# Kernel optimization log

Hardware: AMD Instinct MI355X
Metric: run time of the kernel (lower is better)

Reference implementation:

```python
import jax, jax.numpy as jnp
import numpy as np

DIM = 2048
K = 8                 # top_k
M = 16                # max_transients
BIND_FRAC = 0.15
BETA = 0.05
GAMMA = 0.9
LIFETIME = 5
B, T = 64, 256

_iu, _ju = np.triu_indices(K, k=1)   # row-major: matches torch's (ii outer, jj inner) loop order
IU = jnp.asarray(_iu, jnp.int32)
JU = jnp.asarray(_ju, jnp.int32)


def _renorm(s):
    n = jnp.sqrt(jnp.sum(jnp.abs(s) ** 2, axis=-1, keepdims=True))
    return s / jnp.maximum(n, 1e-8)


def setup_inputs() -> dict:
    key = jax.random.key(0)
    ks = jax.random.split(key, 5)
    return {
        "x": jax.random.normal(ks[0], (B, T, DIM), jnp.float32),
        "tape_re": jax.random.normal(ks[1], (DIM,), jnp.float32) / np.sqrt(DIM).astype(np.float32),
        "tape_im": jax.random.normal(ks[2], (DIM,), jnp.float32) / np.sqrt(DIM).astype(np.float32),
        "eta_param": jnp.asarray(0.1, jnp.float32),
        "torque_bias_re": jax.random.normal(ks[3], (DIM,), jnp.float32) * 0.01,
        "torque_bias_im": jax.random.normal(ks[4], (DIM,), jnp.float32) * 0.01,
    }


def _per_batch(h, s, ti, tj, mre, mim, cnt, eta, tbias):
    """One timestep for one batch element. s: [D] complex64, transients: 5 arrays of [M]."""
    c = h * s                               # Hadamard reception
    _, top_idx = jax.lax.top_k(jnp.abs(c), K)
    top_c = c[top_idx]
    tm = jnp.abs(top_c)
    ph = jnp.angle(top_c)
    # co-resonance scores for the K*(K-1)/2 pairs; torch detaches via .item()
    score = jax.lax.stop_gradient(tm[IU] * tm[JU] * jnp.cos(ph[IU] - ph[JU]))
    pos = score > 0
    n_pos = jnp.sum(pos.astype(jnp.int32))
    n_bind = jnp.maximum(1, (n_pos.astype(jnp.float32) * BIND_FRAC).astype(jnp.int32))
    sorted_desc = -jnp.sort(-jnp.where(pos, score, -jnp.inf))
    theta_idx = jnp.minimum(n_bind - 1, jnp.maximum(n_pos - 1, 0))
    theta = sorted_desc[theta_idx]
    bind = (score >= theta) & (n_pos > 0)   # theta>0 so only positive scores pass

    ci = top_idx[IU]
    cj = top_idx[JU]
    prod = s[ci] * s[cj]
    mnew = jax.lax.stop_gradient(BETA * prod / jnp.maximum(jnp.abs(prod), 1e-8))  # torch detaches via .item()

    def step(tr, inp):
        ti, tj, mre, mim, cnt = tr
        ci_p, cj_p, do, mr, mi = inp
        active = cnt > 0
        match = active & (((ti == ci_p) & (tj == cj_p)) | ((ti == cj_p) & (tj == ci_p)))
        has_match = jnp.any(match)
        midx = jnp.argmax(match)
        free = ~active
        has_free = jnp.any(free)
        fidx = jnp.argmax(free)
        refresh = do & has_match
        insert = do & (~has_match) & has_free
        cnt = jnp.where(refresh, cnt.at[midx].set(LIFETIME), cnt)
        ti = jnp.where(insert, ti.at[fidx].set(ci_p), ti)
        tj = jnp.where(insert, tj.at[fidx].set(cj_p), tj)
        mre = jnp.where(insert, mre.at[fidx].set(mr), mre)
        mim = jnp.where(insert, mim.at[fidx].set(mi), mim)
        cnt = jnp.where(insert, cnt.at[fidx].set(LIFETIME), cnt)
        return (ti, tj, mre, mim, cnt), None

    (ti, tj, mre, mim, cnt), _ = jax.lax.scan(
        step, (ti, tj, mre, mim, cnt), (ci, cj, bind, mnew.real, mnew.imag))

    # decay all transients
    mre = mre * GAMMA
    mim = mim * GAMMA
    cnt = cnt - 1
    alive = (cnt > 0) & (jnp.sqrt(mre * mre + mim * mim) > 1e-6)
    cnt = jnp.where(alive, cnt, 0)
    mre = jnp.where(alive, mre, 0.0)
    mim = jnp.where(alive, mim, 0.0)

    # augment state with transients (scatter-add to both endpoints)
    s_re = s.real.at[ti].add(0.1 * mre).at[tj].add(0.1 * mre)
    s_im = s.imag.at[ti].add(0.1 * mim).at[tj].add(0.1 * mim)
    s_aug = jax.lax.complex(s_re, s_im)

    c_aug = h * s_aug
    re_c = c_aug.real
    im_c = c_aug.imag
    res_mask = ((re_c > 1e-6) & (jnp.abs(im_c) < re_c)).astype(jnp.float32)
    tor_mask = ((re_c < -1e-6) | (jnp.abs(im_c) >= jnp.abs(re_c))).astype(jnp.float32)
    orth_mask = 1.0 - res_mask - tor_mask
    update = eta * (c_aug * (1.0 - orth_mask) + tor_mask * tbias)
    s_new = _renorm(s + update)
    return s_new, ti, tj, mre, mim, cnt


def _forward(x, tape_re, tape_im, eta_param, torque_bias_re, torque_bias_im):
    Bb, Tt, D = x.shape
    s0 = _renorm(jax.lax.complex(tape_re, tape_im)[None, :])
    s0 = jnp.broadcast_to(s0, (Bb, D))
    eta = jnp.abs(eta_param)
    tbias = jax.lax.complex(torque_bias_re, torque_bias_im)
    ti0 = jnp.zeros((Bb, M), jnp.int32)
    tj0 = jnp.zeros((Bb, M), jnp.int32)
    mre0 = jnp.zeros((Bb, M), jnp.float32)
    mim0 = jnp.zeros((Bb, M), jnp.float32)
    cnt0 = jnp.zeros((Bb, M), jnp.int32)

    step_b = jax.vmap(_per_batch, in_axes=(0, 0, 0, 0, 0, 0, 0, None, None))

    def time_step(carry, h_t):
        s, ti, tj, mre, mim, cnt = carry
        s, ti, tj, mre, mim, cnt = step_b(h_t, s, ti, tj, mre, mim, cnt, eta, tbias)
        return (s, ti, tj, mre, mim, cnt), jnp.abs(s)

    _, outs = jax.lax.scan(time_step, (s0, ti0, tj0, mre0, mim0, cnt0),
                           jnp.transpose(x, (1, 0, 2)))  # [T,B,D]
    return jnp.transpose(outs, (1, 0, 2))                # [B,T,D]


def reference(x, tape_re, tape_im, eta_param, torque_bias_re, torque_bias_im):
    return _forward(x, tape_re, tape_im, eta_param, torque_bias_re, torque_bias_im)
```

## Files before the change

kernel.cpp:

```cpp
#include <hip/hip_runtime.h>
#include <math.h>

#define DIM_ 2048
#define KTOP 8
#define MSLOT 16
#define TSTEPS 256
#define NB 64
#define NTHREADS 320
#define NWORK 256
#define EPT 8

static_assert(NWORK * EPT == DIM_, "mapping");

#define DPP0(src, ctrl, rm) __builtin_amdgcn_update_dpp(0, (src), (ctrl), (rm), 0xf, true)

__device__ __forceinline__ void ced(double &a, double &b) {
  double mx = fmax(a, b);
  b = fmin(a, b);
  a = mx;
}

__device__ __forceinline__ void sort8_desc(double k[8]) {
  ced(k[0],k[1]); ced(k[2],k[3]); ced(k[4],k[5]); ced(k[6],k[7]);
  ced(k[0],k[2]); ced(k[1],k[3]); ced(k[4],k[6]); ced(k[5],k[7]);
  ced(k[1],k[2]); ced(k[5],k[6]);
  ced(k[0],k[4]); ced(k[1],k[5]); ced(k[2],k[6]); ced(k[3],k[7]);
  ced(k[2],k[4]); ced(k[3],k[5]);
  ced(k[1],k[2]); ced(k[3],k[4]); ced(k[5],k[6]);
}

template <int CTRL, int RM>
__device__ __forceinline__ void merge_level(double k[8]) {
  double b[8];
#pragma unroll
  for (int i = 0; i < 8; i++) {
    int lo = DPP0(__double2loint(k[i]), CTRL, RM);
    int hi = DPP0(__double2hiint(k[i]), CTRL, RM);
    b[i] = __hiloint2double(hi, lo);
  }
#pragma unroll
  for (int i = 0; i < 8; i++) k[i] = fmax(k[i], b[7 - i]);
  ced(k[0],k[4]); ced(k[1],k[5]); ced(k[2],k[6]); ced(k[3],k[7]);
  ced(k[0],k[2]); ced(k[1],k[3]); ced(k[4],k[6]); ced(k[5],k[7]);
  ced(k[0],k[1]); ced(k[2],k[3]); ced(k[4],k[5]); ced(k[6],k[7]);
}

#define FMAX_STAGE(x, ctrl, rm)                                                \
  x = fmaxf(x, __int_as_float(DPP0(__float_as_int(x), ctrl, rm)))
#define FADD_STAGE(x, ctrl, rm)                                                \
  x = x + __int_as_float(DPP0(__float_as_int(x), ctrl, rm))

__device__ __forceinline__ float wave_max_f32(float x) {
  FMAX_STAGE(x, 0x111, 0xf);
  FMAX_STAGE(x, 0x112, 0xf);
  FMAX_STAGE(x, 0x114, 0xf);
  FMAX_STAGE(x, 0x118, 0xf);
  FMAX_STAGE(x, 0x142, 0xa);
  FMAX_STAGE(x, 0x143, 0xc);
  return x;
}
__device__ __forceinline__ float wave_sum_f32(float x) {
  FADD_STAGE(x, 0x111, 0xf);
  FADD_STAGE(x, 0x112, 0xf);
  FADD_STAGE(x, 0x114, 0xf);
  FADD_STAGE(x, 0x118, 0xf);
  FADD_STAGE(x, 0x142, 0xa);
  FADD_STAGE(x, 0x143, 0xc);
  return x;
}
__device__ __forceinline__ int rl63(int v) {
  return __builtin_amdgcn_readlane(v, 63);
}

__global__ void __launch_bounds__(NTHREADS)
me_fused(const float *__restrict__ x, const float *__restrict__ tape_re,
         const float *__restrict__ tape_im, const float *__restrict__ eta_param,
         const float *__restrict__ tbias_re, const float *__restrict__ tbias_im,
         float *__restrict__ out) {
  __shared__ float4 sc4[DIM_];
  __shared__ float2 dxy[DIM_];
  __shared__ unsigned long long cand_lds[4 * KTOP];
  __shared__ float red_sh[4];

  const int tid = threadIdx.x;
  const int lane = tid & 63;
  const int wid = tid >> 6;
  const int wtid = tid - 64;
  const int b = blockIdx.x;

  const float eta = fabsf(eta_param[0]);

  float vre[EPT], vim[EPT], tbre_[EPT], tbim_[EPT];
  float hcur[EPT], hnext[EPT];
  const float *xb = x + (size_t)b * TSTEPS * DIM_;

  if (wid > 0) {
    float acc = 0.f;
#pragma unroll
    for (int j = 0; j < EPT; j++) {
      int e = wtid + NWORK * j;
      float a = tape_re[e], c2 = tape_im[e];
      vre[j] = a; vim[j] = c2;
      tbre_[j] = tbias_re[e]; tbim_[j] = tbias_im[e];
      hcur[j] = xb[e]; hnext[j] = hcur[j];
      acc += a * a + c2 * c2;
    }
    float ws = wave_sum_f32(acc);
    if (lane == 63) red_sh[wid - 1] = ws;
  }

  int s_ti = 0, s_tj = 0, s_cnt = 0;
  float s_mre = 0.f, s_mim = 0.f;

  __syncthreads();

  for (int t = 0; t < TSTEPS; t++) {
    if (wid > 0) {
      double key[EPT];
#pragma unroll
      for (int j = 0; j < EPT; j++) {
        int e = wtid + NWORK * j;
        float h = hcur[j];
        float cr = h * vre[j], ci = h * vim[j];
        float av = sqrtf(cr * cr + ci * ci);
        key[j] = __hiloint2double(__float_as_int(av), ~e);
        sc4[e] = make_float4(h, vre[j], vim[j], 0.f);
        dxy[e] = make_float2(0.f, 0.f);
      }
      sort8_desc(key);
      merge_level<0x111, 0xf>(key);
      merge_level<0x112, 0xf>(key);
      merge_level<0x114, 0xf>(key);
      merge_level<0x118, 0xf>(key);
      merge_level<0x142, 0xa>(key);
      merge_level<0x143, 0xc>(key);
      if (lane == 63) {
#pragma unroll
        for (int r = 0; r < KTOP; r++)
          cand_lds[(wid - 1) * KTOP + r] =
              (unsigned long long)__double_as_longlong(key[r]);
      }
    }
    __syncthreads();

    float ivn;
    {
      float tot = red_sh[0] + red_sh[1] + red_sh[2] + red_sh[3];
      ivn = 1.f / fmaxf(sqrtf(tot), 1e-8f);
    }

    float osr[EPT], osi[EPT];

    if (wid == 0) {
      double c[8];
#pragma unroll
      for (int r = 0; r < KTOP; r++) {
        unsigned long long v = (lane < 4) ? cand_lds[lane * KTOP + r] : 0ull;
        c[r] = __longlong_as_double((long long)v);
      }
      merge_level<0x111, 0xf>(c);
      merge_level<0x112, 0xf>(c);
      int top[KTOP];
#pragma unroll
      for (int r = 0; r < KTOP; r++)
        top[r] = ~__builtin_amdgcn_readlane(__double2loint(c[r]), 3);

      int pi = (lane < 28) ? lane : 27;
      int ii = 0, base = 0;
      if (pi >= 7)  { ii = 1; base = 7;  }
      if (pi >= 13) { ii = 2; base = 13; }
      if (pi >= 18) { ii = 3; base = 18; }
      if (pi >= 22) { ii = 4; base = 22; }
      if (pi >= 25) { ii = 5; base = 25; }
      if (pi >= 27) { ii = 6; base = 27; }
      int jj = ii + 1 + (pi - base);
      int gi = top[0];
      if (ii == 1) gi = top[1];
      if (ii == 2) gi = top[2];
      if (ii == 3) gi = top[3];
      if (ii == 4) gi = top[4];
      if (ii == 5) gi = top[5];
      if (ii == 6) gi = top[6];
      int gj = top[1];
      if (jj == 2) gj = top[2];
      if (jj == 3) gj = top[3];
      if (jj == 4) gj = top[4];
      if (jj == 5) gj = top[5];
      if (jj == 6) gj = top[6];
      if (jj == 7) gj = top[7];

      float4 c4i = sc4[gi], c4j = sc4[gj];
      float sri = c4i.y * ivn, sii2 = c4i.z * ivn;
      float srj = c4j.y * ivn, sij = c4j.z * ivn;
      float cri = c4i.x * sri, cii = c4i.x * sii2;
      float crj = c4j.x * srj, cij = c4j.x * sij;
      float score = cri * crj + cii * cij;
      bool valid = (lane < 28);
      bool pos = valid && (score > 0.f);
      unsigned long long posmask = __ballot(pos);
      int npos = __popcll(posmask);
      float pr = sri * srj - sii2 * sij;
      float pq = sri * sij + sii2 * srj;
      float ap = fmaxf(sqrtf(pr * pr + pq * pq), 1e-8f);
      float mr = (0.05f * pr) / ap, mi = (0.05f * pq) / ap;

      unsigned long long bmask = 0ull;
      if (npos > 0) {
        int nbind = (int)((float)npos * 0.15f);
        if (nbind < 1) nbind = 1;
        float val = pos ? score : -__builtin_inff();
        float th = 0.f;
        for (int k2 = 0; k2 < nbind; ++k2) {
          float mx = wave_max_f32(val);
          th = __int_as_float(rl63(__float_as_int(mx)));
          if (k2 + 1 < nbind) {
            unsigned long long em = __ballot(val == th);
            if (lane == (int)__builtin_ctzll(em)) val = -__builtin_inff();
          }
        }
        bool bind = valid && (score >= th);
        bmask = __ballot(bind);
      }
      while (bmask) {
        int pp = (int)__builtin_ctzll(bmask);
        bmask &= bmask - 1;
        int pci = __builtin_amdgcn_readlane(gi, pp);
        int pcj = __builtin_amdgcn_readlane(gj, pp);
        int pmr = __builtin_amdgcn_readlane(__float_as_int(mr), pp);
        int pmi = __builtin_amdgcn_readlane(__float_as_int(mi), pp);
        bool isslot = (lane < MSLOT);
        bool match = isslot && (s_cnt > 0) &&
                     ((s_ti == pci && s_tj == pcj) ||
                      (s_ti == pcj && s_tj == pci));
        unsigned long long mm = __ballot(match);
        if (mm != 0ull) {
          if (lane == (int)__builtin_ctzll(mm)) s_cnt = 5;
        } else {
          unsigned long long fm = __ballot(isslot && s_cnt <= 0);
          if (fm != 0ull && lane == (int)__builtin_ctzll(fm)) {
            s_ti = pci; s_tj = pcj;
            s_mre = __int_as_float(pmr); s_mim = __int_as_float(pmi);
            s_cnt = 5;
          }
        }
      }
      if (lane < MSLOT) {
        s_mre *= 0.9f; s_mim *= 0.9f; s_cnt -= 1;
        bool alive = (s_cnt > 0) &&
                     (sqrtf(s_mre * s_mre + s_mim * s_mim) > 1e-6f);
        if (!alive) { s_cnt = 0; s_mre = 0.f; s_mim = 0.f; }
        atomicAdd(&dxy[s_ti].x, 0.1f * s_mre);
        atomicAdd(&dxy[s_tj].x, 0.1f * s_mre);
        atomicAdd(&dxy[s_ti].y, 0.1f * s_mim);
        atomicAdd(&dxy[s_tj].y, 0.1f * s_mim);
      }
    } else {
      if (t + 1 < TSTEPS) {
        const float *xr = xb + (size_t)(t + 1) * DIM_;
#pragma unroll
        for (int j = 0; j < EPT; j++) hnext[j] = xr[wtid + NWORK * j];
      }
      if (t > 0) {
        float *op = out + ((size_t)b * TSTEPS + (t - 1)) * DIM_;
#pragma unroll
        for (int j = 0; j < EPT; j++) {
          float sr = vre[j] * ivn, si = vim[j] * ivn;
          op[wtid + NWORK * j] = sqrtf(sr * sr + si * si);
        }
      }
#pragma unroll
      for (int j = 0; j < EPT; j++) {
        float sri = vre[j] * ivn, sii2 = vim[j] * ivn;
        osr[j] = sri; osi[j] = sii2;
        float h = hcur[j];
        float car = h * sri, cai = h * sii2;
        bool res = (car > 1e-6f) && (fabsf(cai) < car);
        bool tor = (car < -1e-6f) || (fabsf(cai) >= fabsf(car));
        float m1 = (res || tor) ? 1.f : 0.f;
        float mt = tor ? 1.f : 0.f;
        float ur = eta * (car * m1 + mt * tbre_[j]);
        float ui = eta * (cai * m1 + mt * tbim_[j]);
        vre[j] = sri + ur; vim[j] = sii2 + ui;
      }
    }
    __syncthreads();

    if (wid > 0) {
      float2 dd[EPT];
#pragma unroll
      for (int j = 0; j < EPT; j++) dd[j] = dxy[wtid + NWORK * j];
      float acc2 = 0.f;
#pragma unroll
      for (int j = 0; j < EPT; j++) {
        if (dd[j].x != 0.f || dd[j].y != 0.f) {
          float ar = osr[j] + dd[j].x, ai = osi[j] + dd[j].y;
          float h = hcur[j];
          float car = h * ar, cai = h * ai;
          bool res = (car > 1e-6f) && (fabsf(cai) < car);
          bool tor = (car < -1e-6f) || (fabsf(cai) >= fabsf(car));
          float m1 = (res || tor) ? 1.f : 0.f;
          float mt = tor ? 1.f : 0.f;
          float ur = eta * (car * m1 + mt * tbre_[j]);
          float ui = eta * (cai * m1 + mt * tbim_[j]);
          vre[j] = osr[j] + ur; vim[j] = osi[j] + ui;
        }
        acc2 += vre[j] * vre[j] + vim[j] * vim[j];
      }
      float ws = wave_sum_f32(acc2);
      if (lane == 63) red_sh[wid - 1] = ws;
#pragma unroll
      for (int j = 0; j < EPT; j++) hcur[j] = hnext[j];
    }
  }

  __syncthreads();
  if (wid > 0) {
    float tot = red_sh[0] + red_sh[1] + red_sh[2] + red_sh[3];
    float ivnF = 1.f / fmaxf(sqrtf(tot), 1e-8f);
    float *op = out + ((size_t)b * TSTEPS + (TSTEPS - 1)) * DIM_;
#pragma unroll
    for (int j = 0; j < EPT; j++) {
      float sr = vre[j] * ivnF, si = vim[j] * ivnF;
      op[wtid + NWORK * j] = sqrtf(sr * sr + si * si);
    }
  }
}

extern "C" void kernel_launch(void *const *d_in, const int *in_sizes, int n_in,
                              void *d_out, int out_size, void *d_ws,
                              size_t ws_size, hipStream_t stream) {
  const float *x = (const float *)d_in[0];
  const float *tre = (const float *)d_in[1];
  const float *tim = (const float *)d_in[2];
  const float *eta = (const float *)d_in[3];
  const float *tbre = (const float *)d_in[4];
  const float *tbim = (const float *)d_in[5];
  float *out = (float *)d_out;
  me_fused<<<NB, NTHREADS, 0, stream>>>(x, tre, tim, eta, tbre, tbim, out);
}
```

Before: 1.058 ms.

## Pack two batch rows per block and pass top-k values via candidate slots

Each block now processes two batch elements with 640 threads in place of one with 320, halving the grid to 32 blocks. The full sc4 staging array is replaced by a small cand_val table filled by the worker lanes that own the top-8 candidates, so the control wave reads precomputed products directly. dxy is zeroed once up front and then only at the transient slots, and barriers become plain s_barrier with an LDS waitcnt. This cuts per-step LDS traffic and barrier cost, but the two batch rows now share each barrier and only 32 CUs are busy.

```diff
diff --git a/kernel.cpp b/kernel.cpp
--- a/kernel.cpp
+++ b/kernel.cpp
@@ -1,14 +1,15 @@
 #include <hip/hip_runtime.h>
 #include <math.h>
 
-#define DIM_ 2048
 #define KTOP 8
 #define MSLOT 16
 #define TSTEPS 256
-#define NB 64
-#define NTHREADS 320
+#define NBPB 2
+#define NB 32
+#define NTHREADS 640
 #define NWORK 256
 #define EPT 8
+#define DIM_ 2048
 
 static_assert(NWORK * EPT == DIM_, "mapping");
 
@@ -72,33 +73,44 @@
   return __builtin_amdgcn_readlane(v, 63);
 }
 
+__device__ __forceinline__ void barrier_lds() {
+  asm volatile("s_waitcnt lgkmcnt(0)\n\ts_barrier" ::: "memory");
+}
+
 __global__ void __launch_bounds__(NTHREADS)
 me_fused(const float *__restrict__ x, const float *__restrict__ tape_re,
          const float *__restrict__ tape_im, const float *__restrict__ eta_param,
          const float *__restrict__ tbias_re, const float *__restrict__ tbias_im,
          float *__restrict__ out) {
-  __shared__ float4 sc4[DIM_];
-  __shared__ float2 dxy[DIM_];
-  __shared__ unsigned long long cand_lds[4 * KTOP];
-  __shared__ float red_sh[4];
+  __shared__ float2 dxy[NBPB][DIM_];
+  __shared__ unsigned long long cand_key[NBPB][4 * KTOP];
+  __shared__ float4 cand_val[NBPB][4 * KTOP];
+  __shared__ float red_sh[NBPB][4];
 
   const int tid = threadIdx.x;
   const int lane = tid & 63;
   const int wid = tid >> 6;
-  const int wtid = tid - 64;
-  const int b = blockIdx.x;
+  const int q = (wid >= 5) ? 1 : 0;
+  const int gw = wid - 5 * q;
+  const int wtid = (gw - 1) * 64 + lane;
+  const int b = blockIdx.x * NBPB + q;
 
   const float eta = fabsf(eta_param[0]);
+
+  for (int i = tid; i < NBPB * DIM_; i += NTHREADS)
+    ((float2 *)dxy)[i] = make_float2(0.f, 0.f);
 
   float vre[EPT], vim[EPT], tbre_[EPT], tbim_[EPT];
   float hcur[EPT], hnext[EPT];
+  int elo[EPT];
   const float *xb = x + (size_t)b * TSTEPS * DIM_;
 
-  if (wid > 0) {
+  if (gw > 0) {
     float acc = 0.f;
 #pragma unroll
     for (int j = 0; j < EPT; j++) {
       int e = wtid + NWORK * j;
+      elo[j] = (2047 - e) << 5;
       float a = tape_re[e], c2 = tape_im[e];
       vre[j] = a; vim[j] = c2;
       tbre_[j] = tbias_re[e]; tbim_[j] = tbias_im[e];
@@ -106,26 +118,25 @@
       acc += a * a + c2 * c2;
     }
     float ws = wave_sum_f32(acc);
-    if (lane == 63) red_sh[wid - 1] = ws;
+    if (lane == 63) red_sh[q][gw - 1] = ws;
   }
 
   int s_ti = 0, s_tj = 0, s_cnt = 0;
   float s_mre = 0.f, s_mim = 0.f;
 
-  __syncthreads();
+  barrier_lds();
 
   for (int t = 0; t < TSTEPS; t++) {
-    if (wid > 0) {
+    if (gw > 0) {
       double key[EPT];
+      float cr8[EPT], ci8[EPT];
 #pragma unroll
       for (int j = 0; j < EPT; j++) {
-        int e = wtid + NWORK * j;
         float h = hcur[j];
         float cr = h * vre[j], ci = h * vim[j];
+        cr8[j] = cr; ci8[j] = ci;
         float av = sqrtf(cr * cr + ci * ci);
-        key[j] = __hiloint2double(__float_as_int(av), ~e);
-        sc4[e] = make_float4(h, vre[j], vim[j], 0.f);
-        dxy[e] = make_float2(0.f, 0.f);
+        key[j] = __hiloint2double(__float_as_int(av), elo[j]);
       }
       sort8_desc(key);
       merge_level<0x111, 0xf>(key);
@@ -134,37 +145,59 @@
       merge_level<0x118, 0xf>(key);
       merge_level<0x142, 0xa>(key);
       merge_level<0x143, 0xc>(key);
+      int blo[KTOP];
+#pragma unroll
+      for (int r = 0; r < KTOP; r++)
+        blo[r] = __builtin_amdgcn_readlane(__double2loint(key[r]), 63);
       if (lane == 63) {
 #pragma unroll
-        for (int r = 0; r < KTOP; r++)
-          cand_lds[(wid - 1) * KTOP + r] =
-              (unsigned long long)__double_as_longlong(key[r]);
-      }
-    }
-    __syncthreads();
-
-    float ivn;
-    {
-      float tot = red_sh[0] + red_sh[1] + red_sh[2] + red_sh[3];
+        for (int r = 0; r < KTOP; r++) {
+          int slot = (gw - 1) * KTOP + r;
+          cand_key[q][slot] =
+              (((unsigned long long)(unsigned)__double2hiint(key[r])) << 32) |
+              (unsigned)(__double2loint(key[r]) | slot);
+        }
+      }
+#pragma unroll
+      for (int j = 0; j < EPT; j++) {
+        int m = -1;
+#pragma unroll
+        for (int r = 0; r < KTOP; r++) m = (blo[r] == elo[j]) ? r : m;
+        if (m >= 0)
+          cand_val[q][(gw - 1) * KTOP + m] =
+              make_float4(cr8[j], ci8[j], vre[j], vim[j]);
+      }
+    }
+    barrier_lds();
+
+    float ivn = 0.f;
+    if (gw > 0) {
+      float tot = red_sh[q][0] + red_sh[q][1] + red_sh[q][2] + red_sh[q][3];
       ivn = 1.f / fmaxf(sqrtf(tot), 1e-8f);
     }
 
     float osr[EPT], osi[EPT];
 
-    if (wid == 0) {
-      double c[8];
+    if (gw == 0) {
+      if (lane < MSLOT) {
+        dxy[q][s_ti] = make_float2(0.f, 0.f);
+        dxy[q][s_tj] = make_float2(0.f, 0.f);
+      }
+      double c[KTOP];
 #pragma unroll
       for (int r = 0; r < KTOP; r++) {
-        unsigned long long v = (lane < 4) ? cand_lds[lane * KTOP + r] : 0ull;
+        unsigned long long v = (lane < 4) ? cand_key[q][lane * KTOP + r] : 0ull;
         c[r] = __longlong_as_double((long long)v);
       }
       merge_level<0x111, 0xf>(c);
       merge_level<0x112, 0xf>(c);
-      int top[KTOP];
-#pragma unroll
-      for (int r = 0; r < KTOP; r++)
-        top[r] = ~__builtin_amdgcn_readlane(__double2loint(c[r]), 3);
-
+      int gidx[KTOP], slt[KTOP];
+#pragma unroll
+      for (int r = 0; r < KTOP; r++) {
+        int lo = __builtin_amdgcn_readlane(__double2loint(c[r]), 3);
+        gidx[r] = 2047 - ((lo >> 5) & 0x7ff);
+        slt[r] = lo & 31;
+      }
       int pi = (lane < 28) ? lane : 27;
       int ii = 0, base = 0;
       if (pi >= 7)  { ii = 1; base = 7;  }
@@ -174,35 +207,31 @@
       if (pi >= 25) { ii = 5; base = 25; }
       if (pi >= 27) { ii = 6; base = 27; }
       int jj = ii + 1 + (pi - base);
-      int gi = top[0];
-      if (ii == 1) gi = top[1];
-      if (ii == 2) gi = top[2];
-      if (ii == 3) gi = top[3];
-      if (ii == 4) gi = top[4];
-      if (ii == 5) gi = top[5];
-      if (ii == 6) gi = top[6];
-      int gj = top[1];
-      if (jj == 2) gj = top[2];
-      if (jj == 3) gj = top[3];
-      if (jj == 4) gj = top[4];
-      if (jj == 5) gj = top[5];
-      if (jj == 6) gj = top[6];
-      if (jj == 7) gj = top[7];
-
-      float4 c4i = sc4[gi], c4j = sc4[gj];
-      float sri = c4i.y * ivn, sii2 = c4i.z * ivn;
-      float srj = c4j.y * ivn, sij = c4j.z * ivn;
-      float cri = c4i.x * sri, cii = c4i.x * sii2;
-      float crj = c4j.x * srj, cij = c4j.x * sij;
-      float score = cri * crj + cii * cij;
+      int gi = gidx[0], sli = slt[0];
+      if (ii == 1) { gi = gidx[1]; sli = slt[1]; }
+      if (ii == 2) { gi = gidx[2]; sli = slt[2]; }
+      if (ii == 3) { gi = gidx[3]; sli = slt[3]; }
+      if (ii == 4) { gi = gidx[4]; sli = slt[4]; }
+      if (ii == 5) { gi = gidx[5]; sli = slt[5]; }
+      if (ii == 6) { gi = gidx[6]; sli = slt[6]; }
+      int gj = gidx[1], slj = slt[1];
+      if (jj == 2) { gj = gidx[2]; slj = slt[2]; }
+      if (jj == 3) { gj = gidx[3]; slj = slt[3]; }
+      if (jj == 4) { gj = gidx[4]; slj = slt[4]; }
+      if (jj == 5) { gj = gidx[5]; slj = slt[5]; }
+      if (jj == 6) { gj = gidx[6]; slj = slt[6]; }
+      if (jj == 7) { gj = gidx[7]; slj = slt[7]; }
+
+      float4 c4i = cand_val[q][sli], c4j = cand_val[q][slj];
+      float score = c4i.x * c4j.x + c4i.y * c4j.y;
       bool valid = (lane < 28);
       bool pos = valid && (score > 0.f);
       unsigned long long posmask = __ballot(pos);
       int npos = __popcll(posmask);
-      float pr = sri * srj - sii2 * sij;
-      float pq = sri * sij + sii2 * srj;
-      float ap = fmaxf(sqrtf(pr * pr + pq * pq), 1e-8f);
-      float mr = (0.05f * pr) / ap, mi = (0.05f * pq) / ap;
+      float pr = c4i.z * c4j.z - c4i.w * c4j.w;
+      float pq2 = c4i.z * c4j.w + c4i.w * c4j.z;
+      float ap = fmaxf(sqrtf(pr * pr + pq2 * pq2), 1e-8f);
+      float mr = (0.05f * pr) / ap, mi = (0.05f * pq2) / ap;
 
       unsigned long long bmask = 0ull;
       if (npos > 0) {
@@ -249,10 +278,10 @@
         bool alive = (s_cnt > 0) &&
                      (sqrtf(s_mre * s_mre + s_mim * s_mim) > 1e-6f);
         if (!alive) { s_cnt = 0; s_mre = 0.f; s_mim = 0.f; }
-        atomicAdd(&dxy[s_ti].x, 0.1f * s_mre);
-        atomicAdd(&dxy[s_tj].x, 0.1f * s_mre);
-        atomicAdd(&dxy[s_ti].y, 0.1f * s_mim);
-        atomicAdd(&dxy[s_tj].y, 0.1f * s_mim);
+        atomicAdd(&dxy[q][s_ti].x, 0.1f * s_mre);
+        atomicAdd(&dxy[q][s_tj].x, 0.1f * s_mre);
+        atomicAdd(&dxy[q][s_ti].y, 0.1f * s_mim);
+        atomicAdd(&dxy[q][s_tj].y, 0.1f * s_mim);
       }
     } else {
       if (t + 1 < TSTEPS) {
@@ -283,12 +312,12 @@
         vre[j] = sri + ur; vim[j] = sii2 + ui;
       }
     }
-    __syncthreads();
-
-    if (wid > 0) {
+    barrier_lds();
+
+    if (gw > 0) {
       float2 dd[EPT];
 #pragma unroll
-      for (int j = 0; j < EPT; j++) dd[j] = dxy[wtid + NWORK * j];
+      for (int j = 0; j < EPT; j++) dd[j] = dxy[q][wtid + NWORK * j];
       float acc2 = 0.f;
 #pragma unroll
       for (int j = 0; j < EPT; j++) {
@@ -307,15 +336,15 @@
         acc2 += vre[j] * vre[j] + vim[j] * vim[j];
       }
       float ws = wave_sum_f32(acc2);
-      if (lane == 63) red_sh[wid - 1] = ws;
+      if (lane == 63) red_sh[q][gw - 1] = ws;
 #pragma unroll
       for (int j = 0; j < EPT; j++) hcur[j] = hnext[j];
     }
   }
 
-  __syncthreads();
-  if (wid > 0) {
-    float tot = red_sh[0] + red_sh[1] + red_sh[2] + red_sh[3];
+  barrier_lds();
+  if (gw > 0) {
+    float tot = red_sh[q][0] + red_sh[q][1] + red_sh[q][2] + red_sh[q][3];
     float ivnF = 1.f / fmaxf(sqrtf(tot), 1e-8f);
     float *op = out + ((size_t)b * TSTEPS + (TSTEPS - 1)) * DIM_;
 #pragma unroll
```

After: 2.034 ms. 1.92x slower.
